# Optimization experiments

Measured on AMD Instinct MI355X. Metric: run time of the kernel, lower is better.

Reference implementation:

```python
import jax, jax.numpy as jnp
import numpy as np

B, N, C, H = 4, 4096, 512, 16  # batch, seq (=input_resolution), dim, num_heads


def setup_inputs() -> dict:
    key = jax.random.key(0)
    k1, k2, k3, k4 = jax.random.split(key, 4)
    x = jax.random.normal(k1, (B, N, C), jnp.float32)
    Wqk = jax.random.normal(k2, (C, 2 * C), jnp.float32) / np.sqrt(C)
    bqk = jnp.zeros((2 * C,), jnp.float32)
    lepe_w = jax.random.normal(k3, (C, 1, 3), jnp.float32) * 0.1  # depthwise conv, groups=C
    lepe_b = jnp.zeros((C,), jnp.float32)
    return {"x": x, "Wqk": Wqk, "bqk": bqk, "lepe_w": lepe_w, "lepe_b": lepe_b}


def _rope(x):
    # x: [b, n, c]; 1D RoPE over the sequence axis, k_max = c // 2 pairs.
    b, n, c = x.shape
    k_max = c // 2
    theta = 1.0 / (10000.0 ** (jnp.arange(k_max, dtype=jnp.float32) / k_max))
    ang = jnp.arange(n, dtype=jnp.float32)[:, None] * theta  # [n, k_max]
    cos, sin = jnp.cos(ang), jnp.sin(ang)
    xr, xi = x[..., 0::2], x[..., 1::2]  # consecutive (re, im) pairs
    out = jnp.stack([xr * cos - xi * sin, xr * sin + xi * cos], axis=-1)
    return out.reshape(b, n, c)


def reference(x, Wqk, bqk, lepe_w, lepe_b):
    b, n, c = x.shape
    h = H
    d = c // h
    qk = x @ Wqk + bqk  # [b, n, 2c]
    q = jax.nn.elu(qk[..., :c]) + 1.0
    k = jax.nn.elu(qk[..., c:]) + 1.0
    q_rope = _rope(q).reshape(b, n, h, d).transpose(0, 2, 1, 3)  # [b,h,n,d]
    k_rope = _rope(k).reshape(b, n, h, d).transpose(0, 2, 1, 3)
    qh = q.reshape(b, n, h, d).transpose(0, 2, 1, 3)
    kh = k.reshape(b, n, h, d).transpose(0, 2, 1, 3)
    v = x.reshape(b, n, h, d).transpose(0, 2, 1, 3)
    # normalizer z = 1 / (q . mean_n(k) + eps)
    kmean = kh.mean(axis=2)  # [b,h,d]
    z = 1.0 / (jnp.einsum('bhnd,bhd->bhn', qh, kmean) + 1e-6)  # [b,h,n]
    # kv = (k_rope^T / sqrt(n)) @ (v / sqrt(n))
    kv = jnp.einsum('bhnd,bhne->bhde', k_rope, v) / n  # [b,h,d,d]
    out = jnp.einsum('bhnd,bhde->bhne', q_rope, kv) * z[..., None]  # [b,h,n,d]
    out = out.transpose(0, 2, 1, 3).reshape(b, n, c)
    # LePE: depthwise conv1d over sequence on v (v reassembled == x)
    vt = x.transpose(0, 2, 1)  # [b, c, n]
    lepe = jax.lax.conv_general_dilated(
        vt, lepe_w, window_strides=(1,), padding=((1, 1),),
        feature_group_count=c, dimension_numbers=('NCH', 'OIH', 'NCH'))
    lepe = lepe + lepe_b[None, :, None]
    return out + lepe.transpose(0, 2, 1)
```

## Files before the change

### kernel.cpp

```cpp
#include <hip/hip_runtime.h>

typedef unsigned short u16;
typedef u16   u16x8 __attribute__((ext_vector_type(8)));
typedef short s16x8 __attribute__((ext_vector_type(8)));
typedef float f32x4 __attribute__((ext_vector_type(4)));

__device__ __forceinline__ float b2f(u16 u) {
    return __uint_as_float(((unsigned)u) << 16);
}
__device__ __forceinline__ u16 f2b(float f) {
    unsigned x = __float_as_uint(f);
    x += 0x7fffu + ((x >> 16) & 1u);
    return (u16)(x >> 16);
}
__device__ __forceinline__ void gload_lds(const u16* g, u16* l) {
    __builtin_amdgcn_global_load_lds(
        (const __attribute__((address_space(1))) unsigned int*)g,
        (__attribute__((address_space(3))) unsigned int*)l, 16, 0, 0);
}

#define THETA_SCALE 0.05190512648261f

__global__ __launch_bounds__(256)
void k_prep(const float* __restrict__ X, u16* __restrict__ Xb,
            const float* __restrict__ W, u16* __restrict__ WT,
            float* __restrict__ kvz) {
    if (blockIdx.x < 4096) {
        size_t i = (size_t)(blockIdx.x * 256 + threadIdx.x) * 8;
        float4 a = *(const float4*)(X + i);
        float4 b = *(const float4*)(X + i + 4);
        u16x8 r;
        r[0] = f2b(a.x); r[1] = f2b(a.y); r[2] = f2b(a.z); r[3] = f2b(a.w);
        r[4] = f2b(b.x); r[5] = f2b(b.y); r[6] = f2b(b.z); r[7] = f2b(b.w);
        *(u16x8*)(Xb + i) = r;
    } else if (blockIdx.x < 4608) {
        __shared__ float tile[32][33];
        int bid = blockIdx.x - 4096;
        int c0 = (bid & 31) * 32;
        int r0 = (bid >> 5) * 32;
        int tx = threadIdx.x & 31;
        int ty = threadIdx.x >> 5;
        #pragma unroll
        for (int i = 0; i < 4; ++i) {
            int r = ty + i * 8;
            tile[r][tx] = W[(size_t)(r0 + r) * 1024 + c0 + tx];
        }
        __syncthreads();
        #pragma unroll
        for (int i = 0; i < 4; ++i) {
            int r = ty + i * 8;
            WT[(size_t)(c0 + r) * 512 + r0 + tx] = f2b(tile[tx][r]);
        }
    } else {
        size_t i = (size_t)(blockIdx.x - 4608) * 1024 + threadIdx.x * 4;
        *(float4*)(kvz + i) = make_float4(0.f, 0.f, 0.f, 0.f);
    }
}

__global__ __launch_bounds__(256)
void k_gemm(const u16* __restrict__ Xb, const u16* __restrict__ WT,
            const float* __restrict__ bqk,
            u16* __restrict__ Qb, u16* __restrict__ Kb) {
    __shared__ u16 As[128 * 64];
    __shared__ u16 Bs[128 * 64];
    const int t = threadIdx.x;
    const int m0 = blockIdx.x * 128;
    const int n0 = blockIdx.y * 128;
    const int lane = t & 63;
    const int wave = t >> 6;
    const int wm = (wave >> 1) * 64;
    const int wn = (wave & 1) * 64;
    const int quad = lane >> 4;
    const int l16 = lane & 15;
    const int lr = lane >> 3;
    const int cg = ((lane & 7) ^ lr) * 8;

    f32x4 acc[4][4];
    f32x4 zero4 = {0.f, 0.f, 0.f, 0.f};
    #pragma unroll
    for (int i = 0; i < 4; ++i)
        #pragma unroll
        for (int j = 0; j < 4; ++j) acc[i][j] = zero4;

    for (int k0 = 0; k0 < 512; k0 += 64) {
        __syncthreads();
        #pragma unroll
        for (int g = 0; g < 4; ++g) {
            int r0 = wave * 32 + g * 8;
            size_t ga = (size_t)(m0 + r0 + lr) * 512 + k0 + cg;
            size_t gb = (size_t)(n0 + r0 + lr) * 512 + k0 + cg;
            gload_lds(Xb + ga, &As[r0 * 64]);
            gload_lds(WT + gb, &Bs[r0 * 64]);
        }
        __syncthreads();
        #pragma unroll
        for (int ks = 0; ks < 64; ks += 32) {
            const int cbase = quad + (ks >> 3);
            s16x8 a4[4], b4[4];
            #pragma unroll
            for (int i = 0; i < 4; ++i) {
                int row = wm + i * 16 + l16;
                a4[i] = *(const s16x8*)&As[row * 64 + ((cbase ^ (row & 7)) * 8)];
            }
            #pragma unroll
            for (int j = 0; j < 4; ++j) {
                int row = wn + j * 16 + l16;
                b4[j] = *(const s16x8*)&Bs[row * 64 + ((cbase ^ (row & 7)) * 8)];
            }
            #pragma unroll
            for (int i = 0; i < 4; ++i)
                #pragma unroll
                for (int j = 0; j < 4; ++j)
                    acc[i][j] = __builtin_amdgcn_mfma_f32_16x16x32_bf16(
                        a4[i], b4[j], acc[i][j], 0, 0, 0);
        }
    }

    u16* O = (n0 < 512) ? Qb : Kb;
    #pragma unroll
    for (int i = 0; i < 4; ++i)
        #pragma unroll
        for (int j = 0; j < 4; ++j) {
            int col = n0 + wn + j * 16 + l16;
            float bias = bqk[col];
            int gc = col & 511;
            #pragma unroll
            for (int r = 0; r < 4; ++r) {
                int grow = m0 + wm + i * 16 + quad * 4 + r;
                float v = acc[i][j][r] + bias;
                v = v > 0.f ? v + 1.f : __expf(v);
                O[(size_t)grow * 512 + gc] = f2b(v);
            }
        }
}

__global__ __launch_bounds__(256)
void k_kv(const u16* __restrict__ Kb, const u16* __restrict__ Xb,
          float* __restrict__ kvbuf, float* __restrict__ ksum) {
    const int bh = blockIdx.x;
    const int b = bh >> 4, h = bh & 15;
    const int nb = blockIdx.y * 512;
    __shared__ u16 krT[32 * 72];
    __shared__ u16 vT[32 * 72];
    __shared__ float red[64 * 36];
    const int t = threadIdx.x;
    const int row = t >> 2;
    const int c8 = (t & 3) * 8;
    const int rot_w = 16 * ((c8 >> 3) & 3);
    const int lane = t & 63;
    const int wave = t >> 6;
    const int quad = lane >> 4;
    const int l16 = lane & 15;
    const int dq = (wave >> 1) * 16;
    const int eq = (wave & 1) * 16;
    const int ca = dq + l16;
    const int cb2 = eq + l16;
    const int rot_a = 16 * ((ca >> 3) & 3);
    const int rot_b = 16 * ((cb2 >> 3) & 3);

    float ksl[8] = {0, 0, 0, 0, 0, 0, 0, 0};
    f32x4 acc = {0.f, 0.f, 0.f, 0.f};

    float th[4];
    #pragma unroll
    for (int p = 0; p < 4; ++p)
        th[p] = exp2f(-THETA_SCALE * (float)(h * 16 + (c8 >> 1) + p));

    for (int pass = 0; pass < 8; ++pass) {
        int n = nb + pass * 64 + row;
        size_t base = (size_t)(b * 4096 + n) * 512 + h * 32 + c8;
        u16x8 k8 = *(const u16x8*)(Kb + base);
        u16x8 v8 = *(const u16x8*)(Xb + base);
        float kf[8], kr[8];
        #pragma unroll
        for (int j = 0; j < 8; ++j) kf[j] = b2f(k8[j]);
        #pragma unroll
        for (int p = 0; p < 4; ++p) {
            float sv, cv;
            sincosf((float)n * th[p], &sv, &cv);
            kr[2 * p]     = kf[2 * p] * cv - kf[2 * p + 1] * sv;
            kr[2 * p + 1] = kf[2 * p] * sv + kf[2 * p + 1] * cv;
        }
        #pragma unroll
        for (int j = 0; j < 8; ++j) ksl[j] += kf[j];
        if (pass) __syncthreads();
        int colw = (row + rot_w) & 63;
        #pragma unroll
        for (int j = 0; j < 8; ++j) {
            krT[(c8 + j) * 72 + colw] = f2b(kr[j]);
            vT[(c8 + j) * 72 + colw] = v8[j];
        }
        __syncthreads();
        #pragma unroll
        for (int ks = 0; ks < 64; ks += 32) {
            s16x8 a4 = *(const s16x8*)&krT[ca * 72 + ((ks + quad * 8 + rot_a) & 63)];
            s16x8 b4 = *(const s16x8*)&vT[cb2 * 72 + ((ks + quad * 8 + rot_b) & 63)];
            acc = __builtin_amdgcn_mfma_f32_16x16x32_bf16(a4, b4, acc, 0, 0, 0);
        }
    }

    #pragma unroll
    for (int r = 0; r < 4; ++r)
        atomicAdd(&kvbuf[(size_t)bh * 1024 + (dq + quad * 4 + r) * 32 + eq + l16],
                  acc[r]);

    __syncthreads();
    *(float4*)&red[row * 36 + c8]     = make_float4(ksl[0], ksl[1], ksl[2], ksl[3]);
    *(float4*)&red[row * 36 + c8 + 4] = make_float4(ksl[4], ksl[5], ksl[6], ksl[7]);
    __syncthreads();
    if (t < 32) {
        float s = 0.f;
        for (int r = 0; r < 64; ++r) s += red[r * 36 + t];
        atomicAdd(&ksum[bh * 32 + t], s);
    }
}

__global__ __launch_bounds__(256)
void k_out(const u16* __restrict__ Qb, const u16* __restrict__ Xb,
           const float* __restrict__ kvbuf, const float* __restrict__ ksum,
           const float* __restrict__ lw, const float* __restrict__ lb,
           float* __restrict__ OUT) {
    const int b = blockIdx.x >> 6;
    const int nb = (blockIdx.x & 63) * 64;
    const int hbase = blockIdx.y * 4;
    __shared__ float kv_s[32 * 36];
    __shared__ float qr_s[64 * 36];
    __shared__ float ks_s[32];
    __shared__ float z_s[64];
    const int t = threadIdx.x;
    const int row = t >> 2;
    const int c4 = t & 3;
    const int e0 = c4 * 8;
    const float invN = 1.f / 4096.f;
    const int n = nb + row;
    const size_t rowbase = (size_t)(b * 4096 + n) * 512;

    for (int hh = 0; hh < 4; ++hh) {
        const int h = hbase + hh;
        const int bh = b * 16 + h;
        if (hh) __syncthreads();
        #pragma unroll
        for (int i = 0; i < 4; ++i) {
            int id = t + i * 256;
            kv_s[(id >> 5) * 36 + (id & 31)] = kvbuf[(size_t)bh * 1024 + id] * invN;
        }
        if (t < 32) ks_s[t] = ksum[bh * 32 + t] * invN;
        __syncthreads();

        u16x8 q8 = *(const u16x8*)(Qb + rowbase + h * 32 + e0);
        float qf[8];
        #pragma unroll
        for (int j = 0; j < 8; ++j) qf[j] = b2f(q8[j]);
        float part = 0.f;
        #pragma unroll
        for (int j = 0; j < 8; ++j) part += qf[j] * ks_s[e0 + j];
        float qr[8];
        #pragma unroll
        for (int p = 0; p < 4; ++p) {
            float th = exp2f(-THETA_SCALE * (float)(h * 16 + c4 * 4 + p));
            float sv, cv;
            sincosf((float)n * th, &sv, &cv);
            qr[2 * p]     = qf[2 * p] * cv - qf[2 * p + 1] * sv;
            qr[2 * p + 1] = qf[2 * p] * sv + qf[2 * p + 1] * cv;
        }
        *(float4*)&qr_s[row * 36 + e0]     = make_float4(qr[0], qr[1], qr[2], qr[3]);
        *(float4*)&qr_s[row * 36 + e0 + 4] = make_float4(qr[4], qr[5], qr[6], qr[7]);
        part += __shfl_xor(part, 1);
        part += __shfl_xor(part, 2);
        if (c4 == 0) z_s[row] = 1.f / (part + 1e-6f);
        __syncthreads();

        float o[8] = {0, 0, 0, 0, 0, 0, 0, 0};
        #pragma unroll 4
        for (int dd = 0; dd < 32; ++dd) {
            float qd = qr_s[row * 36 + dd];
            const float4 k0v = *(const float4*)&kv_s[dd * 36 + e0];
            const float4 k1v = *(const float4*)&kv_s[dd * 36 + e0 + 4];
            o[0] += qd * k0v.x; o[1] += qd * k0v.y; o[2] += qd * k0v.z; o[3] += qd * k0v.w;
            o[4] += qd * k1v.x; o[5] += qd * k1v.y; o[6] += qd * k1v.z; o[7] += qd * k1v.w;
        }
        const float z = z_s[row];

        const int cb = h * 32 + e0;
        u16x8 xc = *(const u16x8*)(Xb + rowbase + cb);
        u16x8 xm = {0, 0, 0, 0, 0, 0, 0, 0};
        u16x8 xp = {0, 0, 0, 0, 0, 0, 0, 0};
        if (n > 0)    xm = *(const u16x8*)(Xb + rowbase - 512 + cb);
        if (n < 4095) xp = *(const u16x8*)(Xb + rowbase + 512 + cb);
        float rv[8];
        #pragma unroll
        for (int j = 0; j < 8; ++j) {
            int c = cb + j;
            float lep = b2f(xm[j]) * lw[c * 3] +
                        b2f(xc[j]) * lw[c * 3 + 1] +
                        b2f(xp[j]) * lw[c * 3 + 2] + lb[c];
            rv[j] = o[j] * z + lep;
        }
        float* Of = OUT + rowbase + cb;
        *(float4*)Of       = make_float4(rv[0], rv[1], rv[2], rv[3]);
        *(float4*)(Of + 4) = make_float4(rv[4], rv[5], rv[6], rv[7]);
    }
}

extern "C" void kernel_launch(void* const* d_in, const int* in_sizes, int n_in,
                              void* d_out, int out_size, void* d_ws, size_t ws_size,
                              hipStream_t stream) {
    const float* x   = (const float*)d_in[0];
    const float* Wqk = (const float*)d_in[1];
    const float* bqk = (const float*)d_in[2];
    const float* lw  = (const float*)d_in[3];
    const float* lb  = (const float*)d_in[4];
    float* out = (float*)d_out;

    char* w = (char*)d_ws;
    u16* Kb      = (u16*)w;   w += (size_t)16384 * 512 * 2;
    u16* Qb      = (u16*)w;   w += (size_t)16384 * 512 * 2;
    u16* Xb      = (u16*)w;   w += (size_t)16384 * 512 * 2;
    u16* WT      = (u16*)w;   w += (size_t)1024 * 512 * 2;
    float* kvbuf = (float*)w; w += (size_t)64 * 1024 * 4;
    float* ksum  = (float*)w;

    k_prep<<<4674, 256, 0, stream>>>(x, Xb, Wqk, WT, kvbuf);
    k_gemm<<<dim3(128, 8), 256, 0, stream>>>(Xb, WT, bqk, Qb, Kb);
    k_kv<<<dim3(64, 8), 256, 0, stream>>>(Kb, Xb, kvbuf, ksum);
    k_out<<<dim3(256, 4), 256, 0, stream>>>(Qb, Xb, kvbuf, ksum, lw, lb, out);
}
```

Before: 147.9 us.

## Fuse K RoPE, key-sum and KV reduction into the QK GEMM epilogue

```diff
diff --git a/kernel.cpp b/kernel.cpp
--- a/kernel.cpp
+++ b/kernel.cpp
@@ -1,6 +1,7 @@
 #include <hip/hip_runtime.h>
 
 typedef unsigned short u16;
+typedef u16   u16x4 __attribute__((ext_vector_type(4)));
 typedef u16   u16x8 __attribute__((ext_vector_type(8)));
 typedef short s16x8 __attribute__((ext_vector_type(8)));
 typedef float f32x4 __attribute__((ext_vector_type(4)));
@@ -59,10 +60,13 @@
 
 __global__ __launch_bounds__(256)
 void k_gemm(const u16* __restrict__ Xb, const u16* __restrict__ WT,
-            const float* __restrict__ bqk,
-            u16* __restrict__ Qb, u16* __restrict__ Kb) {
-    __shared__ u16 As[128 * 64];
-    __shared__ u16 Bs[128 * 64];
+            const float* __restrict__ bqk, u16* __restrict__ Qb,
+            float* __restrict__ kvbuf, float* __restrict__ ksum) {
+    __shared__ u16 shm[128 * 128];
+    __shared__ u16 vTs[32 * 128];
+    __shared__ float ksl[128];
+    u16* As = shm;
+    u16* Bs = shm + 128 * 64;
     const int t = threadIdx.x;
     const int m0 = blockIdx.x * 128;
     const int n0 = blockIdx.y * 128;
@@ -116,102 +120,124 @@
         }
     }
 
-    u16* O = (n0 < 512) ? Qb : Kb;
-    #pragma unroll
-    for (int i = 0; i < 4; ++i)
-        #pragma unroll
-        for (int j = 0; j < 4; ++j) {
-            int col = n0 + wn + j * 16 + l16;
-            float bias = bqk[col];
-            int gc = col & 511;
+    if (n0 < 512) {
+        #pragma unroll
+        for (int i = 0; i < 4; ++i)
+            #pragma unroll
+            for (int j = 0; j < 4; ++j) {
+                int col = n0 + wn + j * 16 + l16;
+                float bias = bqk[col];
+                #pragma unroll
+                for (int r = 0; r < 4; ++r) {
+                    int grow = m0 + wm + i * 16 + quad * 4 + r;
+                    float v = acc[i][j][r] + bias;
+                    v = v > 0.f ? v + 1.f : __expf(v);
+                    Qb[(size_t)grow * 512 + col] = f2b(v);
+                }
+            }
+        return;
+    }
+
+    const int batch = m0 >> 12;
+    const int h0 = (n0 - 512) >> 5;
+    if (t < 128) ksl[t] = 0.f;
+
+    float csum[4];
+    #pragma unroll
+    for (int j = 0; j < 4; ++j) {
+        int gc = (n0 - 512) + wn + j * 16 + l16;
+        float bias = bqk[gc + 512];
+        float s = 0.f;
+        #pragma unroll
+        for (int i = 0; i < 4; ++i)
             #pragma unroll
             for (int r = 0; r < 4; ++r) {
-                int grow = m0 + wm + i * 16 + quad * 4 + r;
                 float v = acc[i][j][r] + bias;
                 v = v > 0.f ? v + 1.f : __expf(v);
-                O[(size_t)grow * 512 + gc] = f2b(v);
-            }
-        }
-}
-
-__global__ __launch_bounds__(256)
-void k_kv(const u16* __restrict__ Kb, const u16* __restrict__ Xb,
-          float* __restrict__ kvbuf, float* __restrict__ ksum) {
-    const int bh = blockIdx.x;
-    const int b = bh >> 4, h = bh & 15;
-    const int nb = blockIdx.y * 512;
-    __shared__ u16 krT[32 * 72];
-    __shared__ u16 vT[32 * 72];
-    __shared__ float red[64 * 36];
-    const int t = threadIdx.x;
-    const int row = t >> 2;
-    const int c8 = (t & 3) * 8;
-    const int rot_w = 16 * ((c8 >> 3) & 3);
-    const int lane = t & 63;
-    const int wave = t >> 6;
-    const int quad = lane >> 4;
-    const int l16 = lane & 15;
-    const int dq = (wave >> 1) * 16;
-    const int eq = (wave & 1) * 16;
-    const int ca = dq + l16;
-    const int cb2 = eq + l16;
-    const int rot_a = 16 * ((ca >> 3) & 3);
-    const int rot_b = 16 * ((cb2 >> 3) & 3);
-
-    float ksl[8] = {0, 0, 0, 0, 0, 0, 0, 0};
-    f32x4 acc = {0.f, 0.f, 0.f, 0.f};
-
-    float th[4];
-    #pragma unroll
-    for (int p = 0; p < 4; ++p)
-        th[p] = exp2f(-THETA_SCALE * (float)(h * 16 + (c8 >> 1) + p));
-
-    for (int pass = 0; pass < 8; ++pass) {
-        int n = nb + pass * 64 + row;
-        size_t base = (size_t)(b * 4096 + n) * 512 + h * 32 + c8;
-        u16x8 k8 = *(const u16x8*)(Kb + base);
-        u16x8 v8 = *(const u16x8*)(Xb + base);
-        float kf[8], kr[8];
-        #pragma unroll
-        for (int j = 0; j < 8; ++j) kf[j] = b2f(k8[j]);
-        #pragma unroll
-        for (int p = 0; p < 4; ++p) {
-            float sv, cv;
-            sincosf((float)n * th[p], &sv, &cv);
-            kr[2 * p]     = kf[2 * p] * cv - kf[2 * p + 1] * sv;
-            kr[2 * p + 1] = kf[2 * p] * sv + kf[2 * p + 1] * cv;
-        }
-        #pragma unroll
-        for (int j = 0; j < 8; ++j) ksl[j] += kf[j];
-        if (pass) __syncthreads();
-        int colw = (row + rot_w) & 63;
-        #pragma unroll
-        for (int j = 0; j < 8; ++j) {
-            krT[(c8 + j) * 72 + colw] = f2b(kr[j]);
-            vT[(c8 + j) * 72 + colw] = v8[j];
-        }
-        __syncthreads();
-        #pragma unroll
-        for (int ks = 0; ks < 64; ks += 32) {
-            s16x8 a4 = *(const s16x8*)&krT[ca * 72 + ((ks + quad * 8 + rot_a) & 63)];
-            s16x8 b4 = *(const s16x8*)&vT[cb2 * 72 + ((ks + quad * 8 + rot_b) & 63)];
-            acc = __builtin_amdgcn_mfma_f32_16x16x32_bf16(a4, b4, acc, 0, 0, 0);
-        }
-    }
-
-    #pragma unroll
-    for (int r = 0; r < 4; ++r)
-        atomicAdd(&kvbuf[(size_t)bh * 1024 + (dq + quad * 4 + r) * 32 + eq + l16],
-                  acc[r]);
-
+                acc[i][j][r] = v;
+                s += v;
+            }
+        csum[j] = s;
+    }
     __syncthreads();
-    *(float4*)&red[row * 36 + c8]     = make_float4(ksl[0], ksl[1], ksl[2], ksl[3]);
-    *(float4*)&red[row * 36 + c8 + 4] = make_float4(ksl[4], ksl[5], ksl[6], ksl[7]);
+    #pragma unroll
+    for (int j = 0; j < 4; ++j)
+        atomicAdd(&ksl[wn + j * 16 + l16], csum[j]);
+
+    const int evenlane = (l16 & 1) == 0;
+    #pragma unroll
+    for (int j = 0; j < 4; ++j) {
+        int gc = (n0 - 512) + wn + j * 16 + l16;
+        float th = exp2f(-THETA_SCALE * (float)(gc >> 1));
+        #pragma unroll
+        for (int i = 0; i < 4; ++i)
+            #pragma unroll
+            for (int r = 0; r < 4; ++r) {
+                int n = ((m0 + wm + i * 16 + quad * 4 + r) & 4095);
+                float k = acc[i][j][r];
+                float p = __shfl_xor(k, 1);
+                float sv, cv;
+                sincosf((float)n * th, &sv, &cv);
+                acc[i][j][r] = evenlane ? (k * cv - p * sv) : (p * sv + k * cv);
+            }
+    }
+
+    #pragma unroll
+    for (int j = 0; j < 4; ++j) {
+        int lc = wn + j * 16 + l16;
+        #pragma unroll
+        for (int i = 0; i < 4; ++i) {
+            int rowb = wm + i * 16 + quad * 4;
+            int phys = lc * 128 + (((rowb >> 3) ^ (lc & 7)) << 3) + (rowb & 7);
+            u16x4 w4;
+            w4[0] = f2b(acc[i][j][0]); w4[1] = f2b(acc[i][j][1]);
+            w4[2] = f2b(acc[i][j][2]); w4[3] = f2b(acc[i][j][3]);
+            *(u16x4*)&shm[phys] = w4;
+        }
+    }
     __syncthreads();
-    if (t < 32) {
-        float s = 0.f;
-        for (int r = 0; r < 64; ++r) s += red[r * 36 + t];
-        atomicAdd(&ksum[bh * 32 + t], s);
+
+    if (t < 128) {
+        int gc = (n0 - 512) + t;
+        atomicAdd(&ksum[(batch * 16 + (gc >> 5)) * 32 + (gc & 31)], ksl[t]);
+    }
+
+    const int vrow = t >> 1;
+    const int vhalf = (t & 1) * 16;
+    for (int hh = 0; hh < 4; ++hh) {
+        if (hh) __syncthreads();
+        {
+            size_t gb = (size_t)(m0 + vrow) * 512 + (n0 - 512) + hh * 32 + vhalf;
+            u16x8 v0 = *(const u16x8*)(Xb + gb);
+            u16x8 v1 = *(const u16x8*)(Xb + gb + 8);
+            #pragma unroll
+            for (int jj = 0; jj < 8; ++jj) {
+                int e0 = vhalf + jj, e1 = vhalf + 8 + jj;
+                vTs[e0 * 128 + (((vrow >> 3) ^ (e0 & 7)) << 3) + (vrow & 7)] = v0[jj];
+                vTs[e1 * 128 + (((vrow >> 3) ^ (e1 & 7)) << 3) + (vrow & 7)] = v1[jj];
+            }
+        }
+        __syncthreads();
+        const int bh = batch * 16 + h0 + hh;
+        #pragma unroll
+        for (int dt = 0; dt < 2; ++dt) {
+            int ac = hh * 32 + dt * 16 + l16;
+            s16x8 a4 = *(const s16x8*)
+                &shm[ac * 128 + ((((wave * 4 + quad)) ^ (ac & 7)) << 3)];
+            #pragma unroll
+            for (int et = 0; et < 2; ++et) {
+                int bc = et * 16 + l16;
+                s16x8 b4 = *(const s16x8*)
+                    &vTs[bc * 128 + ((((wave * 4 + quad)) ^ (bc & 7)) << 3)];
+                f32x4 kvq = __builtin_amdgcn_mfma_f32_16x16x32_bf16(
+                    a4, b4, zero4, 0, 0, 0);
+                #pragma unroll
+                for (int r = 0; r < 4; ++r)
+                    atomicAdd(&kvbuf[(size_t)bh * 1024 +
+                                     (dt * 16 + quad * 4 + r) * 32 + et * 16 + l16],
+                              kvq[r]);
+            }
+        }
     }
 }
 
@@ -313,7 +339,6 @@
     float* out = (float*)d_out;
 
     char* w = (char*)d_ws;
-    u16* Kb      = (u16*)w;   w += (size_t)16384 * 512 * 2;
     u16* Qb      = (u16*)w;   w += (size_t)16384 * 512 * 2;
     u16* Xb      = (u16*)w;   w += (size_t)16384 * 512 * 2;
     u16* WT      = (u16*)w;   w += (size_t)1024 * 512 * 2;
@@ -321,7 +346,6 @@
     float* ksum  = (float*)w;
 
     k_prep<<<4674, 256, 0, stream>>>(x, Xb, Wqk, WT, kvbuf);
-    k_gemm<<<dim3(128, 8), 256, 0, stream>>>(Xb, WT, bqk, Qb, Kb);
-    k_kv<<<dim3(64, 8), 256, 0, stream>>>(Kb, Xb, kvbuf, ksum);
+    k_gemm<<<dim3(128, 8), 256, 0, stream>>>(Xb, WT, bqk, Qb, kvbuf, ksum);
     k_out<<<dim3(256, 4), 256, 0, stream>>>(Qb, Xb, kvbuf, ksum, lw, lb, out);
 }
```

After: 349.8 us. 2.37x slower.

## Fuse four stages into one persistent cooperative kernel with grid syncs

Applied to the files above, without the earlier changes.

```diff
diff --git a/kernel.cpp b/kernel.cpp
--- a/kernel.cpp
+++ b/kernel.cpp
@@ -1,4 +1,7 @@
 #include <hip/hip_runtime.h>
+#include <hip/hip_cooperative_groups.h>
+
+namespace cg = cooperative_groups;
 
 typedef unsigned short u16;
 typedef u16   u16x8 __attribute__((ext_vector_type(8)));
@@ -21,51 +24,45 @@
 
 #define THETA_SCALE 0.05190512648261f
 
-__global__ __launch_bounds__(256)
-void k_prep(const float* __restrict__ X, u16* __restrict__ Xb,
-            const float* __restrict__ W, u16* __restrict__ WT,
-            float* __restrict__ kvz) {
-    if (blockIdx.x < 4096) {
-        size_t i = (size_t)(blockIdx.x * 256 + threadIdx.x) * 8;
-        float4 a = *(const float4*)(X + i);
-        float4 b = *(const float4*)(X + i + 4);
-        u16x8 r;
-        r[0] = f2b(a.x); r[1] = f2b(a.y); r[2] = f2b(a.z); r[3] = f2b(a.w);
-        r[4] = f2b(b.x); r[5] = f2b(b.y); r[6] = f2b(b.z); r[7] = f2b(b.w);
-        *(u16x8*)(Xb + i) = r;
-    } else if (blockIdx.x < 4608) {
-        __shared__ float tile[32][33];
-        int bid = blockIdx.x - 4096;
-        int c0 = (bid & 31) * 32;
-        int r0 = (bid >> 5) * 32;
-        int tx = threadIdx.x & 31;
-        int ty = threadIdx.x >> 5;
-        #pragma unroll
-        for (int i = 0; i < 4; ++i) {
-            int r = ty + i * 8;
-            tile[r][tx] = W[(size_t)(r0 + r) * 1024 + c0 + tx];
-        }
-        __syncthreads();
-        #pragma unroll
-        for (int i = 0; i < 4; ++i) {
-            int r = ty + i * 8;
-            WT[(size_t)(c0 + r) * 512 + r0 + tx] = f2b(tile[tx][r]);
-        }
-    } else {
-        size_t i = (size_t)(blockIdx.x - 4608) * 1024 + threadIdx.x * 4;
-        *(float4*)(kvz + i) = make_float4(0.f, 0.f, 0.f, 0.f);
-    }
-}
-
-__global__ __launch_bounds__(256)
-void k_gemm(const u16* __restrict__ Xb, const u16* __restrict__ WT,
-            const float* __restrict__ bqk,
-            u16* __restrict__ Qb, u16* __restrict__ Kb) {
-    __shared__ u16 As[128 * 64];
-    __shared__ u16 Bs[128 * 64];
-    const int t = threadIdx.x;
-    const int m0 = blockIdx.x * 128;
-    const int n0 = blockIdx.y * 128;
+
+__device__ __forceinline__ void prep_cast(const float* __restrict__ X,
+                                          u16* __restrict__ Xb, int unit, int t) {
+    size_t i = (size_t)unit * 2048 + (size_t)t * 8;
+    float4 a = *(const float4*)(X + i);
+    float4 b = *(const float4*)(X + i + 4);
+    u16x8 r;
+    r[0] = f2b(a.x); r[1] = f2b(a.y); r[2] = f2b(a.z); r[3] = f2b(a.w);
+    r[4] = f2b(b.x); r[5] = f2b(b.y); r[6] = f2b(b.z); r[7] = f2b(b.w);
+    *(u16x8*)(Xb + i) = r;
+}
+
+__device__ __forceinline__ void prep_transpose(const float* __restrict__ W,
+                                               u16* __restrict__ WT,
+                                               float* tile ,
+                                               int bid, int t) {
+    int c0 = (bid & 31) * 32;
+    int r0 = (bid >> 5) * 32;
+    int tx = t & 31;
+    int ty = t >> 5;
+    #pragma unroll
+    for (int i = 0; i < 4; ++i) {
+        int r = ty + i * 8;
+        tile[r * 33 + tx] = W[(size_t)(r0 + r) * 1024 + c0 + tx];
+    }
+    __syncthreads();
+    #pragma unroll
+    for (int i = 0; i < 4; ++i) {
+        int r = ty + i * 8;
+        WT[(size_t)(c0 + r) * 512 + r0 + tx] = f2b(tile[tx * 33 + r]);
+    }
+}
+
+__device__ __forceinline__ void gemm_body(const u16* __restrict__ Xb,
+                                          const u16* __restrict__ WT,
+                                          const float* __restrict__ bqk,
+                                          u16* __restrict__ Qb,
+                                          u16* __restrict__ Kb,
+                                          u16* As, u16* Bs, int m0, int n0, int t) {
     const int lane = t & 63;
     const int wave = t >> 6;
     const int wm = (wave >> 1) * 64;
@@ -73,7 +70,7 @@
     const int quad = lane >> 4;
     const int l16 = lane & 15;
     const int lr = lane >> 3;
-    const int cg = ((lane & 7) ^ lr) * 8;
+    const int cg2 = ((lane & 7) ^ lr) * 8;
 
     f32x4 acc[4][4];
     f32x4 zero4 = {0.f, 0.f, 0.f, 0.f};
@@ -87,8 +84,8 @@
         #pragma unroll
         for (int g = 0; g < 4; ++g) {
             int r0 = wave * 32 + g * 8;
-            size_t ga = (size_t)(m0 + r0 + lr) * 512 + k0 + cg;
-            size_t gb = (size_t)(n0 + r0 + lr) * 512 + k0 + cg;
+            size_t ga = (size_t)(m0 + r0 + lr) * 512 + k0 + cg2;
+            size_t gb = (size_t)(n0 + r0 + lr) * 512 + k0 + cg2;
             gload_lds(Xb + ga, &As[r0 * 64]);
             gload_lds(WT + gb, &Bs[r0 * 64]);
         }
@@ -134,16 +131,13 @@
         }
 }
 
-__global__ __launch_bounds__(256)
-void k_kv(const u16* __restrict__ Kb, const u16* __restrict__ Xb,
-          float* __restrict__ kvbuf, float* __restrict__ ksum) {
-    const int bh = blockIdx.x;
+__device__ __forceinline__ void kv_body(const u16* __restrict__ Kb,
+                                        const u16* __restrict__ Xb,
+                                        float* __restrict__ kvbuf,
+                                        float* __restrict__ ksum,
+                                        u16* krT, u16* vT, float* red,
+                                        int bh, int nb, int npass, int t) {
     const int b = bh >> 4, h = bh & 15;
-    const int nb = blockIdx.y * 512;
-    __shared__ u16 krT[32 * 72];
-    __shared__ u16 vT[32 * 72];
-    __shared__ float red[64 * 36];
-    const int t = threadIdx.x;
     const int row = t >> 2;
     const int c8 = (t & 3) * 8;
     const int rot_w = 16 * ((c8 >> 3) & 3);
@@ -160,13 +154,14 @@
 
     float ksl[8] = {0, 0, 0, 0, 0, 0, 0, 0};
     f32x4 acc = {0.f, 0.f, 0.f, 0.f};
+    f32x4 zero4 = {0.f, 0.f, 0.f, 0.f};
 
     float th[4];
     #pragma unroll
     for (int p = 0; p < 4; ++p)
         th[p] = exp2f(-THETA_SCALE * (float)(h * 16 + (c8 >> 1) + p));
 
-    for (int pass = 0; pass < 8; ++pass) {
+    for (int pass = 0; pass < npass; ++pass) {
         int n = nb + pass * 64 + row;
         size_t base = (size_t)(b * 4096 + n) * 512 + h * 32 + c8;
         u16x8 k8 = *(const u16x8*)(Kb + base);
@@ -183,7 +178,7 @@
         }
         #pragma unroll
         for (int j = 0; j < 8; ++j) ksl[j] += kf[j];
-        if (pass) __syncthreads();
+        __syncthreads();
         int colw = (row + rot_w) & 63;
         #pragma unroll
         for (int j = 0; j < 8; ++j) {
@@ -215,19 +210,16 @@
     }
 }
 
-__global__ __launch_bounds__(256)
-void k_out(const u16* __restrict__ Qb, const u16* __restrict__ Xb,
-           const float* __restrict__ kvbuf, const float* __restrict__ ksum,
-           const float* __restrict__ lw, const float* __restrict__ lb,
-           float* __restrict__ OUT) {
-    const int b = blockIdx.x >> 6;
-    const int nb = (blockIdx.x & 63) * 64;
-    const int hbase = blockIdx.y * 4;
-    __shared__ float kv_s[32 * 36];
-    __shared__ float qr_s[64 * 36];
-    __shared__ float ks_s[32];
-    __shared__ float z_s[64];
-    const int t = threadIdx.x;
+__device__ __forceinline__ void out_body(const u16* __restrict__ Qb,
+                                         const u16* __restrict__ Xb,
+                                         const float* __restrict__ kvbuf,
+                                         const float* __restrict__ ksum,
+                                         const float* __restrict__ lw,
+                                         const float* __restrict__ lb,
+                                         float* __restrict__ OUT,
+                                         float* kv_s, float* qr_s,
+                                         float* ks_s, float* z_s,
+                                         int b, int nb, int hbase, int t) {
     const int row = t >> 2;
     const int c4 = t & 3;
     const int e0 = c4 * 8;
@@ -238,7 +230,7 @@
     for (int hh = 0; hh < 4; ++hh) {
         const int h = hbase + hh;
         const int bh = b * 16 + h;
-        if (hh) __syncthreads();
+        __syncthreads();
         #pragma unroll
         for (int i = 0; i < 4; ++i) {
             int id = t + i * 256;
@@ -300,6 +292,93 @@
         *(float4*)Of       = make_float4(rv[0], rv[1], rv[2], rv[3]);
         *(float4*)(Of + 4) = make_float4(rv[4], rv[5], rv[6], rv[7]);
     }
+}
+
+__global__ __launch_bounds__(256, 4)
+void k_fused(const float* __restrict__ x, const float* __restrict__ Wqk,
+             const float* __restrict__ bqk, const float* __restrict__ lw,
+             const float* __restrict__ lb,
+             u16* __restrict__ Xb, u16* __restrict__ WT,
+             u16* __restrict__ Qb, u16* __restrict__ Kb,
+             float* __restrict__ kvbuf, float* __restrict__ ksum,
+             float* __restrict__ OUT) {
+    __shared__ __align__(16) char smem[32768];
+    const int t = threadIdx.x;
+    const int blk = blockIdx.x;
+    cg::grid_group grid = cg::this_grid();
+
+    #pragma unroll
+    for (int c = 0; c < 4; ++c) prep_cast(x, Xb, blk * 4 + c, t);
+    if (blk < 512) prep_transpose(Wqk, WT, (float*)smem, blk, t);
+    else if (blk < 578) {
+        size_t i = (size_t)(blk - 512) * 1024 + t * 4;
+        *(float4*)(kvbuf + i) = make_float4(0.f, 0.f, 0.f, 0.f);
+    }
+    grid.sync();
+
+    gemm_body(Xb, WT, bqk, Qb, Kb,
+              (u16*)smem, (u16*)(smem + 16384),
+              (blk & 127) * 128, (blk >> 7) * 128, t);
+    grid.sync();
+
+    kv_body(Kb, Xb, kvbuf, ksum,
+            (u16*)smem, (u16*)(smem + 4608), (float*)(smem + 9216),
+            blk & 63, (blk >> 6) * 256, 4, t);
+    grid.sync();
+
+    out_body(Qb, Xb, kvbuf, ksum, lw, lb, OUT,
+             (float*)smem, (float*)(smem + 4608),
+             (float*)(smem + 13824), (float*)(smem + 13952),
+             (blk & 255) >> 6, (blk & 63) * 64, (blk >> 8) * 4, t);
+}
+
+__global__ __launch_bounds__(256)
+void k_prep(const float* __restrict__ X, u16* __restrict__ Xb,
+            const float* __restrict__ W, u16* __restrict__ WT,
+            float* __restrict__ kvz) {
+    if (blockIdx.x < 4096) {
+        prep_cast(X, Xb, blockIdx.x, threadIdx.x);
+    } else if (blockIdx.x < 4608) {
+        __shared__ float tile[32 * 33];
+        prep_transpose(W, WT, tile, blockIdx.x - 4096, threadIdx.x);
+    } else {
+        size_t i = (size_t)(blockIdx.x - 4608) * 1024 + threadIdx.x * 4;
+        *(float4*)(kvz + i) = make_float4(0.f, 0.f, 0.f, 0.f);
+    }
+}
+
+__global__ __launch_bounds__(256)
+void k_gemm(const u16* __restrict__ Xb, const u16* __restrict__ WT,
+            const float* __restrict__ bqk,
+            u16* __restrict__ Qb, u16* __restrict__ Kb) {
+    __shared__ u16 As[128 * 64];
+    __shared__ u16 Bs[128 * 64];
+    gemm_body(Xb, WT, bqk, Qb, Kb, As, Bs,
+              blockIdx.x * 128, blockIdx.y * 128, threadIdx.x);
+}
+
+__global__ __launch_bounds__(256)
+void k_kv(const u16* __restrict__ Kb, const u16* __restrict__ Xb,
+          float* __restrict__ kvbuf, float* __restrict__ ksum) {
+    __shared__ u16 krT[32 * 72];
+    __shared__ u16 vT[32 * 72];
+    __shared__ float red[64 * 36];
+    kv_body(Kb, Xb, kvbuf, ksum, krT, vT, red,
+            blockIdx.x, blockIdx.y * 512, 8, threadIdx.x);
+}
+
+__global__ __launch_bounds__(256)
+void k_out(const u16* __restrict__ Qb, const u16* __restrict__ Xb,
+           const float* __restrict__ kvbuf, const float* __restrict__ ksum,
+           const float* __restrict__ lw, const float* __restrict__ lb,
+           float* __restrict__ OUT) {
+    __shared__ float kv_s[32 * 36];
+    __shared__ float qr_s[64 * 36];
+    __shared__ float ks_s[32];
+    __shared__ float z_s[64];
+    out_body(Qb, Xb, kvbuf, ksum, lw, lb, OUT, kv_s, qr_s, ks_s, z_s,
+             blockIdx.x >> 6, (blockIdx.x & 63) * 64, blockIdx.y * 4,
+             threadIdx.x);
 }
 
 extern "C" void kernel_launch(void* const* d_in, const int* in_sizes, int n_in,
@@ -320,8 +399,15 @@
     float* kvbuf = (float*)w; w += (size_t)64 * 1024 * 4;
     float* ksum  = (float*)w;
 
-    k_prep<<<4674, 256, 0, stream>>>(x, Xb, Wqk, WT, kvbuf);
-    k_gemm<<<dim3(128, 8), 256, 0, stream>>>(Xb, WT, bqk, Qb, Kb);
-    k_kv<<<dim3(64, 8), 256, 0, stream>>>(Kb, Xb, kvbuf, ksum);
-    k_out<<<dim3(256, 4), 256, 0, stream>>>(Qb, Xb, kvbuf, ksum, lw, lb, out);
-}
+    void* args[] = {(void*)&x, (void*)&Wqk, (void*)&bqk, (void*)&lw, (void*)&lb,
+                    (void*)&Xb, (void*)&WT, (void*)&Qb, (void*)&Kb,
+                    (void*)&kvbuf, (void*)&ksum, (void*)&out};
+    hipError_t err = hipLaunchCooperativeKernel(
+        (const void*)k_fused, dim3(1024), dim3(256), args, 0, stream);
+    if (err != hipSuccess) {
+        k_prep<<<4674, 256, 0, stream>>>(x, Xb, Wqk, WT, kvbuf);
+        k_gemm<<<dim3(128, 8), 256, 0, stream>>>(Xb, WT, bqk, Qb, Kb);
+        k_kv<<<dim3(64, 8), 256, 0, stream>>>(Kb, Xb, kvbuf, ksum);
+        k_out<<<dim3(256, 4), 256, 0, stream>>>(Qb, Xb, kvbuf, ksum, lw, lb, out);
+    }
+}
```

New measurement: 540.8 us. 3.66x slower.
